# Performance work log

Measured on AMD Instinct MI355X. Metric: run time of the kernel, lower is better.

Reference implementation:

```python
import jax, jax.numpy as jnp
import numpy as np

B = 262144   # number of (group, item) prediction pairs
M = 16       # max members per group (ragged -> padded)
NU = 100000  # num_users
NI = 50000   # num_items
D = 32       # embedding_dim (hardcoded via torch.zeros([32]))


def setup_inputs() -> dict:
    key = jax.random.key(0)
    ks = jax.random.split(key, 9)
    item_inputs = jax.random.randint(ks[0], (B,), 0, NI)
    member_ids = jax.random.randint(ks[1], (B, M), 0, NU)
    lengths = jax.random.randint(ks[2], (B, 1), 1, M + 1)
    member_mask = jnp.arange(M)[None, :] < lengths  # [B, M] bool, variable group sizes
    user_table = jax.random.normal(ks[3], (NU, D), jnp.float32) * 0.1  # xavier-ish
    item_table = jax.random.normal(ks[4], (NI, D), jnp.float32) * 0.1
    W_bil = jax.random.normal(ks[5], (D, D), jnp.float32)  # nn.Bilinear(D, D, 1) weight[0]
    b_bil = jax.random.normal(ks[6], (1,), jnp.float32) * 0.05
    W1 = jax.random.normal(ks[7], (8, 3 * D), jnp.float32) * 0.05  # Linear(96, 8)
    b1 = jnp.zeros((8,), jnp.float32)
    W2 = jax.random.normal(ks[8], (1, 8), jnp.float32) * 0.05  # Linear(8, 1)
    b2 = jnp.zeros((1,), jnp.float32)
    return {
        "item_inputs": item_inputs, "member_ids": member_ids, "member_mask": member_mask,
        "user_table": user_table, "item_table": item_table,
        "W_bil": W_bil, "b_bil": b_bil, "W1": W1, "b1": b1, "W2": W2, "b2": b2,
    }


def reference(item_inputs, member_ids, member_mask, user_table, item_table,
              W_bil, b_bil, W1, b1, W2, b2):
    item_e = item_table[item_inputs]          # [B, D] gather
    mem_e = user_table[member_ids]            # [B, M, D] gather
    # bilinear attention score per member: m^T W i + b (softmax in original is computed then discarded)
    scores = jnp.einsum('bmd,de,be->bm', mem_e, W_bil, item_e) + b_bil[0]
    w = scores * member_mask.astype(scores.dtype)  # zero out padded members (ragged groups)
    final_user = jnp.einsum('bm,bmd->bd', w, mem_e)  # unnormalized weighted sum of members
    new_embeds = jnp.concatenate([final_user * item_e, final_user, item_e], axis=-1)  # [B, 3D]
    h = jax.nn.relu(new_embeds @ W1.T + b1)
    y = jax.nn.sigmoid(h @ W2.T + b2)          # [B, 1]
    return y
```

## Files before the change

### kernel.cpp

```cpp
#include <hip/hip_runtime.h>
#include <math.h>

#define DD 32
#define MM 16

__device__ __forceinline__ void load8f4(const float* __restrict__ p, float* r) {
    const float4* q = (const float4*)p;
#pragma unroll
    for (int i = 0; i < 8; ++i) {
        float4 v = q[i];
        r[4*i+0] = v.x; r[4*i+1] = v.y; r[4*i+2] = v.z; r[4*i+3] = v.w;
    }
}

__global__ void precompute_item(const float* __restrict__ item_table,
                                const float* __restrict__ W_bil,
                                const float* __restrict__ W1,
                                float* __restrict__ tbl, int NI) {
    int i = blockIdx.x * blockDim.x + threadIdx.x;
    if (i >= NI) return;
    float it[DD];
    load8f4(item_table + (size_t)i * DD, it);
    float* o = tbl + (size_t)i * 40;
#pragma unroll 4
    for (int d = 0; d < DD; ++d) {
        float s = 0.f;
#pragma unroll
        for (int e = 0; e < DD; ++e) s = fmaf(W_bil[d * DD + e], it[e], s);
        o[d] = s;
    }
#pragma unroll
    for (int j = 0; j < 8; ++j) {
        float s = 0.f;
#pragma unroll
        for (int d = 0; d < DD; ++d) s = fmaf(W1[j * 96 + 64 + d], it[d], s);
        o[32 + j] = s;
    }
}

template <bool USE_TBL>
__global__ void bilinear_main(const int* __restrict__ item_inputs,
                              const int* __restrict__ member_ids,
                              const unsigned char* __restrict__ member_mask,
                              const float* __restrict__ user_table,
                              const float* __restrict__ item_table,
                              const float* __restrict__ tbl,
                              const float* __restrict__ W_bil,
                              const float* __restrict__ b_bil,
                              const float* __restrict__ W1,
                              const float* __restrict__ b1,
                              const float* __restrict__ W2,
                              const float* __restrict__ b2,
                              float* __restrict__ out, int Btot) {
    int b = blockIdx.x * blockDim.x + threadIdx.x;
    if (b >= Btot) return;

    int item = item_inputs[b];

    uint4 mv = *(const uint4*)(member_mask + (size_t)b * MM);
    int len = __popc(mv.x & 0x01010101u) + __popc(mv.y & 0x01010101u) +
              __popc(mv.z & 0x01010101u) + __popc(mv.w & 0x01010101u);

    int ids[MM];
    {
        const int4* mp = (const int4*)(member_ids + (size_t)b * MM);
#pragma unroll
        for (int q = 0; q < 4; ++q) {
            int4 v = mp[q];
            ids[4*q+0] = v.x; ids[4*q+1] = v.y; ids[4*q+2] = v.z; ids[4*q+3] = v.w;
        }
    }

    float t[DD];
    float cj[8];
    if (USE_TBL) {
        const float* tb = tbl + (size_t)item * 40;
        load8f4(tb, t);
        float4 c0 = *(const float4*)(tb + 32);
        float4 c1 = *(const float4*)(tb + 36);
        cj[0] = c0.x; cj[1] = c0.y; cj[2] = c0.z; cj[3] = c0.w;
        cj[4] = c1.x; cj[5] = c1.y; cj[6] = c1.z; cj[7] = c1.w;
    } else {
        float it0[DD];
        load8f4(item_table + (size_t)item * DD, it0);
#pragma unroll 4
        for (int d = 0; d < DD; ++d) {
            float s = 0.f;
#pragma unroll
            for (int e = 0; e < DD; ++e) s = fmaf(W_bil[d * DD + e], it0[e], s);
            t[d] = s;
        }
#pragma unroll
        for (int j = 0; j < 8; ++j) {
            float s = 0.f;
#pragma unroll
            for (int d = 0; d < DD; ++d) s = fmaf(W1[j * 96 + 64 + d], it0[d], s);
            cj[j] = s;
        }
    }

    float bb = b_bil[0];
    float fin[DD];
#pragma unroll
    for (int d = 0; d < DD; ++d) fin[d] = 0.f;

    for (int m = 0; m < len; ++m) {
        float me[DD];
        load8f4(user_table + (size_t)ids[m] * DD, me);
        float s = bb;
#pragma unroll
        for (int d = 0; d < DD; ++d) s = fmaf(me[d], t[d], s);
#pragma unroll
        for (int d = 0; d < DD; ++d) fin[d] = fmaf(s, me[d], fin[d]);
    }

    float it[DD];
    load8f4(item_table + (size_t)item * DD, it);

    float h[8];
#pragma unroll
    for (int j = 0; j < 8; ++j) h[j] = cj[j] + b1[j];
#pragma unroll
    for (int d = 0; d < DD; ++d) {
        float f = fin[d];
        float p = f * it[d];
#pragma unroll
        for (int j = 0; j < 8; ++j) {
            h[j] = fmaf(W1[j * 96 + d], p, h[j]);
            h[j] = fmaf(W1[j * 96 + 32 + d], f, h[j]);
        }
    }
    float z = b2[0];
#pragma unroll
    for (int j = 0; j < 8; ++j) {
        float hv = h[j] > 0.f ? h[j] : 0.f;
        z = fmaf(W2[j], hv, z);
    }
    out[b] = 1.f / (1.f + __expf(-z));
}

extern "C" void kernel_launch(void* const* d_in, const int* in_sizes, int n_in,
                              void* d_out, int out_size, void* d_ws, size_t ws_size,
                              hipStream_t stream) {
    const int*           item_inputs = (const int*)d_in[0];
    const int*           member_ids  = (const int*)d_in[1];
    const unsigned char* member_mask = (const unsigned char*)d_in[2];
    const float*         user_table  = (const float*)d_in[3];
    const float*         item_table  = (const float*)d_in[4];
    const float*         W_bil       = (const float*)d_in[5];
    const float*         b_bil       = (const float*)d_in[6];
    const float*         W1          = (const float*)d_in[7];
    const float*         b1          = (const float*)d_in[8];
    const float*         W2          = (const float*)d_in[9];
    const float*         b2          = (const float*)d_in[10];
    float* out = (float*)d_out;

    int Btot = in_sizes[0];
    int NI   = in_sizes[4] / DD;

    bool use_tbl = ws_size >= (size_t)NI * 40 * sizeof(float);
    int blk = 256;
    if (use_tbl) {
        float* tbl = (float*)d_ws;
        precompute_item<<<(NI + blk - 1) / blk, blk, 0, stream>>>(item_table, W_bil, W1, tbl, NI);
        bilinear_main<true><<<(Btot + blk - 1) / blk, blk, 0, stream>>>(
            item_inputs, member_ids, member_mask, user_table, item_table, tbl,
            W_bil, b_bil, W1, b1, W2, b2, out, Btot);
    } else {
        bilinear_main<false><<<(Btot + blk - 1) / blk, blk, 0, stream>>>(
            item_inputs, member_ids, member_mask, user_table, item_table, nullptr,
            W_bil, b_bil, W1, b1, W2, b2, out, Btot);
    }
}
```

Before: 142.4 us.

## Parallelize item precompute per dim, pack item rows, unroll member loop by two

The item precompute kernel now uses one thread per (item, dim) instead of one thread per item, which spreads its work over many more threads. The precomputed row grows to 72 floats and also stores a copy of the item embedding, so the main kernel reads one contiguous row instead of also touching item_table. The member loop handles two members per iteration, issuing both gathers before the math to expose more memory-level parallelism, and dot products use four partial accumulators to shorten dependency chains. The trade-offs are a larger workspace table and higher register pressure in the main kernel.

```diff
diff --git a/kernel.cpp b/kernel.cpp
--- a/kernel.cpp
+++ b/kernel.cpp
@@ -3,6 +3,7 @@
 
 #define DD 32
 #define MM 16
+#define TROW 72
 
 __device__ __forceinline__ void load8f4(const float* __restrict__ p, float* r) {
     const float4* q = (const float4*)p;
@@ -17,41 +18,98 @@
                                 const float* __restrict__ W_bil,
                                 const float* __restrict__ W1,
                                 float* __restrict__ tbl, int NI) {
-    int i = blockIdx.x * blockDim.x + threadIdx.x;
-    if (i >= NI) return;
+    int g = blockIdx.x * blockDim.x + threadIdx.x;
+    if (g >= NI * DD) return;
+    int i = g >> 5;
+    int d = g & (DD - 1);
     float it[DD];
     load8f4(item_table + (size_t)i * DD, it);
-    float* o = tbl + (size_t)i * 40;
-#pragma unroll 4
-    for (int d = 0; d < DD; ++d) {
-        float s = 0.f;
-#pragma unroll
-        for (int e = 0; e < DD; ++e) s = fmaf(W_bil[d * DD + e], it[e], s);
-        o[d] = s;
-    }
-#pragma unroll
-    for (int j = 0; j < 8; ++j) {
-        float s = 0.f;
-#pragma unroll
-        for (int d = 0; d < DD; ++d) s = fmaf(W1[j * 96 + 64 + d], it[d], s);
-        o[32 + j] = s;
-    }
+    const float* w = W_bil + d * DD;
+    float s0 = 0.f, s1 = 0.f, s2 = 0.f, s3 = 0.f;
+#pragma unroll
+    for (int e = 0; e < DD; e += 4) {
+        s0 = fmaf(w[e+0], it[e+0], s0);
+        s1 = fmaf(w[e+1], it[e+1], s1);
+        s2 = fmaf(w[e+2], it[e+2], s2);
+        s3 = fmaf(w[e+3], it[e+3], s3);
+    }
+    float* o = tbl + (size_t)i * TROW;
+    o[d]      = (s0 + s1) + (s2 + s3);
+    o[DD + d] = it[d];
+    if (d < 8) {
+        const float* w1 = W1 + d * 96 + 64;
+        float c0 = 0.f, c1 = 0.f, c2 = 0.f, c3 = 0.f;
+#pragma unroll
+        for (int e = 0; e < DD; e += 4) {
+            c0 = fmaf(w1[e+0], it[e+0], c0);
+            c1 = fmaf(w1[e+1], it[e+1], c1);
+            c2 = fmaf(w1[e+2], it[e+2], c2);
+            c3 = fmaf(w1[e+3], it[e+3], c3);
+        }
+        o[64 + d] = (c0 + c1) + (c2 + c3);
+    }
+}
+
+__device__ __forceinline__ void member1(const float* __restrict__ ut, int id,
+                                        const float* __restrict__ t, float bb,
+                                        float* __restrict__ fin) {
+    float me[DD];
+    load8f4(ut + (size_t)id * DD, me);
+    float s0 = 0.f, s1 = 0.f, s2 = 0.f, s3 = 0.f;
+#pragma unroll
+    for (int d = 0; d < DD; d += 4) {
+        s0 = fmaf(me[d+0], t[d+0], s0);
+        s1 = fmaf(me[d+1], t[d+1], s1);
+        s2 = fmaf(me[d+2], t[d+2], s2);
+        s3 = fmaf(me[d+3], t[d+3], s3);
+    }
+    float s = ((s0 + s1) + (s2 + s3)) + bb;
+#pragma unroll
+    for (int d = 0; d < DD; ++d) fin[d] = fmaf(s, me[d], fin[d]);
+}
+
+__device__ __forceinline__ void member2(const float* __restrict__ ut, int ia, int ib,
+                                        const float* __restrict__ t, float bb,
+                                        float* __restrict__ fin) {
+    float ma[DD], mb[DD];
+    load8f4(ut + (size_t)ia * DD, ma);
+    load8f4(ut + (size_t)ib * DD, mb);
+    float a0 = 0.f, a1 = 0.f, a2 = 0.f, a3 = 0.f;
+    float c0 = 0.f, c1 = 0.f, c2 = 0.f, c3 = 0.f;
+#pragma unroll
+    for (int d = 0; d < DD; d += 4) {
+        a0 = fmaf(ma[d+0], t[d+0], a0);
+        a1 = fmaf(ma[d+1], t[d+1], a1);
+        a2 = fmaf(ma[d+2], t[d+2], a2);
+        a3 = fmaf(ma[d+3], t[d+3], a3);
+        c0 = fmaf(mb[d+0], t[d+0], c0);
+        c1 = fmaf(mb[d+1], t[d+1], c1);
+        c2 = fmaf(mb[d+2], t[d+2], c2);
+        c3 = fmaf(mb[d+3], t[d+3], c3);
+    }
+    float sa = ((a0 + a1) + (a2 + a3)) + bb;
+    float sb = ((c0 + c1) + (c2 + c3)) + bb;
+#pragma unroll
+    for (int d = 0; d < DD; ++d) fin[d] = fmaf(sa, ma[d], fin[d]);
+#pragma unroll
+    for (int d = 0; d < DD; ++d) fin[d] = fmaf(sb, mb[d], fin[d]);
 }
 
 template <bool USE_TBL>
-__global__ void bilinear_main(const int* __restrict__ item_inputs,
-                              const int* __restrict__ member_ids,
-                              const unsigned char* __restrict__ member_mask,
-                              const float* __restrict__ user_table,
-                              const float* __restrict__ item_table,
-                              const float* __restrict__ tbl,
-                              const float* __restrict__ W_bil,
-                              const float* __restrict__ b_bil,
-                              const float* __restrict__ W1,
-                              const float* __restrict__ b1,
-                              const float* __restrict__ W2,
-                              const float* __restrict__ b2,
-                              float* __restrict__ out, int Btot) {
+__global__ __launch_bounds__(256)
+void bilinear_main(const int* __restrict__ item_inputs,
+                   const int* __restrict__ member_ids,
+                   const unsigned char* __restrict__ member_mask,
+                   const float* __restrict__ user_table,
+                   const float* __restrict__ item_table,
+                   const float* __restrict__ tbl,
+                   const float* __restrict__ W_bil,
+                   const float* __restrict__ b_bil,
+                   const float* __restrict__ W1,
+                   const float* __restrict__ b1v,
+                   const float* __restrict__ W2,
+                   const float* __restrict__ b2v,
+                   float* __restrict__ out, int Btot) {
     int b = blockIdx.x * blockDim.x + threadIdx.x;
     if (b >= Btot) return;
 
@@ -72,14 +130,10 @@
     }
 
     float t[DD];
-    float cj[8];
+    const float* tb = nullptr;
     if (USE_TBL) {
-        const float* tb = tbl + (size_t)item * 40;
+        tb = tbl + (size_t)item * TROW;
         load8f4(tb, t);
-        float4 c0 = *(const float4*)(tb + 32);
-        float4 c1 = *(const float4*)(tb + 36);
-        cj[0] = c0.x; cj[1] = c0.y; cj[2] = c0.z; cj[3] = c0.w;
-        cj[4] = c1.x; cj[5] = c1.y; cj[6] = c1.z; cj[7] = c1.w;
     } else {
         float it0[DD];
         load8f4(item_table + (size_t)item * DD, it0);
@@ -90,36 +144,41 @@
             for (int e = 0; e < DD; ++e) s = fmaf(W_bil[d * DD + e], it0[e], s);
             t[d] = s;
         }
+    }
+
+    float bb = b_bil[0];
+    float fin[DD];
+#pragma unroll
+    for (int d = 0; d < DD; ++d) fin[d] = 0.f;
+
+    int m = 0;
+    for (; m + 2 <= len; m += 2)
+        member2(user_table, ids[m], ids[m+1], t, bb, fin);
+    if (m < len)
+        member1(user_table, ids[m], t, bb, fin);
+
+    float it[DD];
+    float cj[8];
+    if (USE_TBL) {
+        load8f4(tb + DD, it);
+        float4 q0 = *(const float4*)(tb + 64);
+        float4 q1 = *(const float4*)(tb + 68);
+        cj[0] = q0.x; cj[1] = q0.y; cj[2] = q0.z; cj[3] = q0.w;
+        cj[4] = q1.x; cj[5] = q1.y; cj[6] = q1.z; cj[7] = q1.w;
+    } else {
+        load8f4(item_table + (size_t)item * DD, it);
 #pragma unroll
         for (int j = 0; j < 8; ++j) {
             float s = 0.f;
 #pragma unroll
-            for (int d = 0; d < DD; ++d) s = fmaf(W1[j * 96 + 64 + d], it0[d], s);
+            for (int d = 0; d < DD; ++d) s = fmaf(W1[j * 96 + 64 + d], it[d], s);
             cj[j] = s;
         }
     }
 
-    float bb = b_bil[0];
-    float fin[DD];
-#pragma unroll
-    for (int d = 0; d < DD; ++d) fin[d] = 0.f;
-
-    for (int m = 0; m < len; ++m) {
-        float me[DD];
-        load8f4(user_table + (size_t)ids[m] * DD, me);
-        float s = bb;
-#pragma unroll
-        for (int d = 0; d < DD; ++d) s = fmaf(me[d], t[d], s);
-#pragma unroll
-        for (int d = 0; d < DD; ++d) fin[d] = fmaf(s, me[d], fin[d]);
-    }
-
-    float it[DD];
-    load8f4(item_table + (size_t)item * DD, it);
-
     float h[8];
 #pragma unroll
-    for (int j = 0; j < 8; ++j) h[j] = cj[j] + b1[j];
+    for (int j = 0; j < 8; ++j) h[j] = cj[j] + b1v[j];
 #pragma unroll
     for (int d = 0; d < DD; ++d) {
         float f = fin[d];
@@ -130,7 +189,7 @@
             h[j] = fmaf(W1[j * 96 + 32 + d], f, h[j]);
         }
     }
-    float z = b2[0];
+    float z = b2v[0];
 #pragma unroll
     for (int j = 0; j < 8; ++j) {
         float hv = h[j] > 0.f ? h[j] : 0.f;
@@ -158,11 +217,11 @@
     int Btot = in_sizes[0];
     int NI   = in_sizes[4] / DD;
 
-    bool use_tbl = ws_size >= (size_t)NI * 40 * sizeof(float);
+    bool use_tbl = ws_size >= (size_t)NI * TROW * sizeof(float);
     int blk = 256;
     if (use_tbl) {
         float* tbl = (float*)d_ws;
-        precompute_item<<<(NI + blk - 1) / blk, blk, 0, stream>>>(item_table, W_bil, W1, tbl, NI);
+        precompute_item<<<(NI * DD + blk - 1) / blk, blk, 0, stream>>>(item_table, W_bil, W1, tbl, NI);
         bilinear_main<true><<<(Btot + blk - 1) / blk, blk, 0, stream>>>(
             item_inputs, member_ids, member_mask, user_table, item_table, tbl,
             W_bil, b_bil, W1, b1, W2, b2, out, Btot);
```

After: 167.1 us. +17.3%, slower.

## Split each batch row across four lanes with shuffle reductions

Applied to the files above, without the earlier changes.

Each (group,item) pair is now handled by four threads, each owning an 8-wide slice of the embedding dimension. Partial dot products for attention scores and the first MLP layer are combined with xor shuffles, and one lane finishes the MLP and writes the output with a nontemporal store. This is meant to cut per-thread register use and raise memory-level parallelism for the random user-table gathers, and adjacent lanes now read contiguous 32-byte chunks of the same row. The cost is extra shuffles per member and redundant loads of the ids and mask in every lane.

```diff
diff --git a/kernel.cpp b/kernel.cpp
--- a/kernel.cpp
+++ b/kernel.cpp
@@ -3,6 +3,7 @@
 
 #define DD 32
 #define MM 16
+#define TROW 40
 
 __device__ __forceinline__ void load8f4(const float* __restrict__ p, float* r) {
     const float4* q = (const float4*)p;
@@ -21,7 +22,7 @@
     if (i >= NI) return;
     float it[DD];
     load8f4(item_table + (size_t)i * DD, it);
-    float* o = tbl + (size_t)i * 40;
+    float* o = tbl + (size_t)i * TROW;
 #pragma unroll 4
     for (int d = 0; d < DD; ++d) {
         float s = 0.f;
@@ -39,104 +40,143 @@
 }
 
 template <bool USE_TBL>
-__global__ void bilinear_main(const int* __restrict__ item_inputs,
-                              const int* __restrict__ member_ids,
-                              const unsigned char* __restrict__ member_mask,
-                              const float* __restrict__ user_table,
-                              const float* __restrict__ item_table,
-                              const float* __restrict__ tbl,
-                              const float* __restrict__ W_bil,
-                              const float* __restrict__ b_bil,
-                              const float* __restrict__ W1,
-                              const float* __restrict__ b1,
-                              const float* __restrict__ W2,
-                              const float* __restrict__ b2,
-                              float* __restrict__ out, int Btot) {
-    int b = blockIdx.x * blockDim.x + threadIdx.x;
+__global__ __launch_bounds__(256)
+void bilinear_main(const int* __restrict__ item_inputs,
+                   const int* __restrict__ member_ids,
+                   const unsigned char* __restrict__ member_mask,
+                   const float* __restrict__ user_table,
+                   const float* __restrict__ item_table,
+                   const float* __restrict__ tbl,
+                   const float* __restrict__ W_bil,
+                   const float* __restrict__ b_bil,
+                   const float* __restrict__ W1,
+                   const float* __restrict__ b1v,
+                   const float* __restrict__ W2,
+                   const float* __restrict__ b2v,
+                   float* __restrict__ out, int Btot) {
+    int tid = blockIdx.x * blockDim.x + threadIdx.x;
+    int b = tid >> 2;
     if (b >= Btot) return;
+    int q  = tid & 3;
+    int ko = q * 8;
 
     int item = item_inputs[b];
 
-    uint4 mv = *(const uint4*)(member_mask + (size_t)b * MM);
+    const uint4 mv = *(const uint4*)(member_mask + (size_t)b * MM);
     int len = __popc(mv.x & 0x01010101u) + __popc(mv.y & 0x01010101u) +
               __popc(mv.z & 0x01010101u) + __popc(mv.w & 0x01010101u);
 
-    int ids[MM];
-    {
-        const int4* mp = (const int4*)(member_ids + (size_t)b * MM);
-#pragma unroll
-        for (int q = 0; q < 4; ++q) {
-            int4 v = mp[q];
-            ids[4*q+0] = v.x; ids[4*q+1] = v.y; ids[4*q+2] = v.z; ids[4*q+3] = v.w;
+    float t[8];
+    if (USE_TBL) {
+        const float4* tp = (const float4*)(tbl + (size_t)item * TROW + ko);
+        float4 a = tp[0], c = tp[1];
+        t[0]=a.x; t[1]=a.y; t[2]=a.z; t[3]=a.w; t[4]=c.x; t[5]=c.y; t[6]=c.z; t[7]=c.w;
+    } else {
+        float itf[DD];
+        load8f4(item_table + (size_t)item * DD, itf);
+#pragma unroll
+        for (int k = 0; k < 8; ++k) {
+            const float* w = W_bil + (ko + k) * DD;
+            float s0 = 0.f, s1 = 0.f, s2 = 0.f, s3 = 0.f;
+#pragma unroll
+            for (int e = 0; e < DD; e += 4) {
+                s0 = fmaf(w[e+0], itf[e+0], s0);
+                s1 = fmaf(w[e+1], itf[e+1], s1);
+                s2 = fmaf(w[e+2], itf[e+2], s2);
+                s3 = fmaf(w[e+3], itf[e+3], s3);
+            }
+            t[k] = (s0 + s1) + (s2 + s3);
         }
     }
 
-    float t[DD];
-    float cj[8];
-    if (USE_TBL) {
-        const float* tb = tbl + (size_t)item * 40;
-        load8f4(tb, t);
-        float4 c0 = *(const float4*)(tb + 32);
-        float4 c1 = *(const float4*)(tb + 36);
-        cj[0] = c0.x; cj[1] = c0.y; cj[2] = c0.z; cj[3] = c0.w;
-        cj[4] = c1.x; cj[5] = c1.y; cj[6] = c1.z; cj[7] = c1.w;
-    } else {
-        float it0[DD];
-        load8f4(item_table + (size_t)item * DD, it0);
-#pragma unroll 4
-        for (int d = 0; d < DD; ++d) {
-            float s = 0.f;
-#pragma unroll
-            for (int e = 0; e < DD; ++e) s = fmaf(W_bil[d * DD + e], it0[e], s);
-            t[d] = s;
+    float bb = b_bil[0];
+    float fin[8];
+#pragma unroll
+    for (int k = 0; k < 8; ++k) fin[k] = 0.f;
+
+    const int* idp = member_ids + (size_t)b * MM;
+    int id = idp[0];
+    for (int m = 0; m < len; ++m) {
+        int idn = idp[(m + 1) & (MM - 1)];
+        const float4* up = (const float4*)(user_table + (size_t)id * DD + ko);
+        float4 a = up[0], c = up[1];
+        float me0 = a.x, me1 = a.y, me2 = a.z, me3 = a.w;
+        float me4 = c.x, me5 = c.y, me6 = c.z, me7 = c.w;
+        float s0 = fmaf(me0, t[0], fmaf(me1, t[1], 0.f));
+        float s1 = fmaf(me2, t[2], fmaf(me3, t[3], 0.f));
+        float s2 = fmaf(me4, t[4], fmaf(me5, t[5], 0.f));
+        float s3 = fmaf(me6, t[6], fmaf(me7, t[7], 0.f));
+        float s = (s0 + s1) + (s2 + s3);
+        s += __shfl_xor(s, 1);
+        s += __shfl_xor(s, 2);
+        s += bb;
+        fin[0] = fmaf(s, me0, fin[0]); fin[1] = fmaf(s, me1, fin[1]);
+        fin[2] = fmaf(s, me2, fin[2]); fin[3] = fmaf(s, me3, fin[3]);
+        fin[4] = fmaf(s, me4, fin[4]); fin[5] = fmaf(s, me5, fin[5]);
+        fin[6] = fmaf(s, me6, fin[6]); fin[7] = fmaf(s, me7, fin[7]);
+        id = idn;
+    }
+
+    const float4* ip = (const float4*)(item_table + (size_t)item * DD + ko);
+    float4 ia = ip[0], ic = ip[1];
+    float it8[8] = {ia.x, ia.y, ia.z, ia.w, ic.x, ic.y, ic.z, ic.w};
+
+    float p8[8];
+#pragma unroll
+    for (int k = 0; k < 8; ++k) p8[k] = fin[k] * it8[k];
+
+    float u[8];
+#pragma unroll
+    for (int j = 0; j < 8; ++j) {
+        const float* wr = W1 + j * 96 + ko;
+        float4 wa0 = *(const float4*)(wr);
+        float4 wa1 = *(const float4*)(wr + 4);
+        float4 wb0 = *(const float4*)(wr + 32);
+        float4 wb1 = *(const float4*)(wr + 36);
+        float x = 0.f, y = 0.f;
+        x = fmaf(wa0.x, p8[0], x); y = fmaf(wb0.x, fin[0], y);
+        x = fmaf(wa0.y, p8[1], x); y = fmaf(wb0.y, fin[1], y);
+        x = fmaf(wa0.z, p8[2], x); y = fmaf(wb0.z, fin[2], y);
+        x = fmaf(wa0.w, p8[3], x); y = fmaf(wb0.w, fin[3], y);
+        x = fmaf(wa1.x, p8[4], x); y = fmaf(wb1.x, fin[4], y);
+        x = fmaf(wa1.y, p8[5], x); y = fmaf(wb1.y, fin[5], y);
+        x = fmaf(wa1.z, p8[6], x); y = fmaf(wb1.z, fin[6], y);
+        x = fmaf(wa1.w, p8[7], x); y = fmaf(wb1.w, fin[7], y);
+        u[j] = x + y;
+    }
+#pragma unroll
+    for (int j = 0; j < 8; ++j) {
+        u[j] += __shfl_xor(u[j], 1);
+        u[j] += __shfl_xor(u[j], 2);
+    }
+
+    if (q == 0) {
+        float cj[8];
+        if (USE_TBL) {
+            const float4* cp = (const float4*)(tbl + (size_t)item * TROW + 32);
+            float4 ca = cp[0], cb = cp[1];
+            cj[0]=ca.x; cj[1]=ca.y; cj[2]=ca.z; cj[3]=ca.w;
+            cj[4]=cb.x; cj[5]=cb.y; cj[6]=cb.z; cj[7]=cb.w;
+        } else {
+            float itf[DD];
+            load8f4(item_table + (size_t)item * DD, itf);
+#pragma unroll
+            for (int j = 0; j < 8; ++j) {
+                float s = 0.f;
+#pragma unroll
+                for (int d = 0; d < DD; ++d) s = fmaf(W1[j * 96 + 64 + d], itf[d], s);
+                cj[j] = s;
+            }
         }
+        float z = b2v[0];
 #pragma unroll
         for (int j = 0; j < 8; ++j) {
-            float s = 0.f;
-#pragma unroll
-            for (int d = 0; d < DD; ++d) s = fmaf(W1[j * 96 + 64 + d], it0[d], s);
-            cj[j] = s;
+            float hv = u[j] + cj[j] + b1v[j];
+            hv = hv > 0.f ? hv : 0.f;
+            z = fmaf(W2[j], hv, z);
         }
-    }
-
-    float bb = b_bil[0];
-    float fin[DD];
-#pragma unroll
-    for (int d = 0; d < DD; ++d) fin[d] = 0.f;
-
-    for (int m = 0; m < len; ++m) {
-        float me[DD];
-        load8f4(user_table + (size_t)ids[m] * DD, me);
-        float s = bb;
-#pragma unroll
-        for (int d = 0; d < DD; ++d) s = fmaf(me[d], t[d], s);
-#pragma unroll
-        for (int d = 0; d < DD; ++d) fin[d] = fmaf(s, me[d], fin[d]);
-    }
-
-    float it[DD];
-    load8f4(item_table + (size_t)item * DD, it);
-
-    float h[8];
-#pragma unroll
-    for (int j = 0; j < 8; ++j) h[j] = cj[j] + b1[j];
-#pragma unroll
-    for (int d = 0; d < DD; ++d) {
-        float f = fin[d];
-        float p = f * it[d];
-#pragma unroll
-        for (int j = 0; j < 8; ++j) {
-            h[j] = fmaf(W1[j * 96 + d], p, h[j]);
-            h[j] = fmaf(W1[j * 96 + 32 + d], f, h[j]);
-        }
-    }
-    float z = b2[0];
-#pragma unroll
-    for (int j = 0; j < 8; ++j) {
-        float hv = h[j] > 0.f ? h[j] : 0.f;
-        z = fmaf(W2[j], hv, z);
-    }
-    out[b] = 1.f / (1.f + __expf(-z));
+        __builtin_nontemporal_store(1.f / (1.f + __expf(-z)), out + b);
+    }
 }
 
 extern "C" void kernel_launch(void* const* d_in, const int* in_sizes, int n_in,
@@ -158,16 +198,17 @@
     int Btot = in_sizes[0];
     int NI   = in_sizes[4] / DD;
 
-    bool use_tbl = ws_size >= (size_t)NI * 40 * sizeof(float);
+    bool use_tbl = ws_size >= (size_t)NI * TROW * sizeof(float);
     int blk = 256;
+    long long nthreads = (long long)Btot * 4;
     if (use_tbl) {
         float* tbl = (float*)d_ws;
         precompute_item<<<(NI + blk - 1) / blk, blk, 0, stream>>>(item_table, W_bil, W1, tbl, NI);
-        bilinear_main<true><<<(Btot + blk - 1) / blk, blk, 0, stream>>>(
+        bilinear_main<true><<<(int)((nthreads + blk - 1) / blk), blk, 0, stream>>>(
             item_inputs, member_ids, member_mask, user_table, item_table, tbl,
             W_bil, b_bil, W1, b1, W2, b2, out, Btot);
     } else {
-        bilinear_main<false><<<(Btot + blk - 1) / blk, blk, 0, stream>>>(
+        bilinear_main<false><<<(int)((nthreads + blk - 1) / blk), blk, 0, stream>>>(
             item_inputs, member_ids, member_mask, user_table, item_table, nullptr,
             W_bil, b_bil, W1, b1, W2, b2, out, Btot);
     }
```

Measured after the change: 154.6 us. 1.09x slower.

## Double-buffer member embedding gathers and split item precompute across two threads

Applied to the files above, without the earlier changes.

The member loop now prefetches the next member's embedding row into a second register buffer while the current one is processed, so gather latency overlaps with the dot product and accumulation. Member ids are read directly from global memory rather than preloaded into a register array. The item precompute kernel uses two threads per item, each computing half of the outputs, and dot products use four independent accumulators to shorten FMA dependency chains. The extra buffer raises register pressure, which may reduce occupancy in this latency-bound gather kernel.

```diff
diff --git a/kernel.cpp b/kernel.cpp
--- a/kernel.cpp
+++ b/kernel.cpp
@@ -3,6 +3,7 @@
 
 #define DD 32
 #define MM 16
+#define TROW 40
 
 __device__ __forceinline__ void load8f4(const float* __restrict__ p, float* r) {
     const float4* q = (const float4*)p;
@@ -17,41 +18,70 @@
                                 const float* __restrict__ W_bil,
                                 const float* __restrict__ W1,
                                 float* __restrict__ tbl, int NI) {
-    int i = blockIdx.x * blockDim.x + threadIdx.x;
+    int g = blockIdx.x * blockDim.x + threadIdx.x;
+    int i = g >> 1, h = g & 1;
     if (i >= NI) return;
     float it[DD];
     load8f4(item_table + (size_t)i * DD, it);
-    float* o = tbl + (size_t)i * 40;
-#pragma unroll 4
-    for (int d = 0; d < DD; ++d) {
-        float s = 0.f;
-#pragma unroll
-        for (int e = 0; e < DD; ++e) s = fmaf(W_bil[d * DD + e], it[e], s);
-        o[d] = s;
-    }
-#pragma unroll
-    for (int j = 0; j < 8; ++j) {
-        float s = 0.f;
-#pragma unroll
-        for (int d = 0; d < DD; ++d) s = fmaf(W1[j * 96 + 64 + d], it[d], s);
-        o[32 + j] = s;
-    }
+    float* o = tbl + (size_t)i * TROW;
+    int d0 = h * 16;
+#pragma unroll
+    for (int k = 0; k < 16; ++k) {
+        const float* w = W_bil + (d0 + k) * DD;
+        float s0 = 0.f, s1 = 0.f, s2 = 0.f, s3 = 0.f;
+#pragma unroll
+        for (int e = 0; e < DD; e += 4) {
+            s0 = fmaf(w[e+0], it[e+0], s0);
+            s1 = fmaf(w[e+1], it[e+1], s1);
+            s2 = fmaf(w[e+2], it[e+2], s2);
+            s3 = fmaf(w[e+3], it[e+3], s3);
+        }
+        o[d0 + k] = (s0 + s1) + (s2 + s3);
+    }
+#pragma unroll
+    for (int jj = 0; jj < 4; ++jj) {
+        int j = h * 4 + jj;
+        const float* w1 = W1 + j * 96 + 64;
+        float c0 = 0.f, c1 = 0.f, c2 = 0.f, c3 = 0.f;
+#pragma unroll
+        for (int e = 0; e < DD; e += 4) {
+            c0 = fmaf(w1[e+0], it[e+0], c0);
+            c1 = fmaf(w1[e+1], it[e+1], c1);
+            c2 = fmaf(w1[e+2], it[e+2], c2);
+            c3 = fmaf(w1[e+3], it[e+3], c3);
+        }
+        o[32 + j] = (c0 + c1) + (c2 + c3);
+    }
+}
+
+__device__ __forceinline__ float dot32(const float* __restrict__ a,
+                                       const float* __restrict__ t) {
+    float s0 = 0.f, s1 = 0.f, s2 = 0.f, s3 = 0.f;
+#pragma unroll
+    for (int d = 0; d < DD; d += 4) {
+        s0 = fmaf(a[d+0], t[d+0], s0);
+        s1 = fmaf(a[d+1], t[d+1], s1);
+        s2 = fmaf(a[d+2], t[d+2], s2);
+        s3 = fmaf(a[d+3], t[d+3], s3);
+    }
+    return (s0 + s1) + (s2 + s3);
 }
 
 template <bool USE_TBL>
-__global__ void bilinear_main(const int* __restrict__ item_inputs,
-                              const int* __restrict__ member_ids,
-                              const unsigned char* __restrict__ member_mask,
-                              const float* __restrict__ user_table,
-                              const float* __restrict__ item_table,
-                              const float* __restrict__ tbl,
-                              const float* __restrict__ W_bil,
-                              const float* __restrict__ b_bil,
-                              const float* __restrict__ W1,
-                              const float* __restrict__ b1,
-                              const float* __restrict__ W2,
-                              const float* __restrict__ b2,
-                              float* __restrict__ out, int Btot) {
+__global__ __launch_bounds__(256)
+void bilinear_main(const int* __restrict__ item_inputs,
+                   const int* __restrict__ member_ids,
+                   const unsigned char* __restrict__ member_mask,
+                   const float* __restrict__ user_table,
+                   const float* __restrict__ item_table,
+                   const float* __restrict__ tbl,
+                   const float* __restrict__ W_bil,
+                   const float* __restrict__ b_bil,
+                   const float* __restrict__ W1,
+                   const float* __restrict__ b1v,
+                   const float* __restrict__ W2,
+                   const float* __restrict__ b2v,
+                   float* __restrict__ out, int Btot) {
     int b = blockIdx.x * blockDim.x + threadIdx.x;
     if (b >= Btot) return;
 
@@ -61,20 +91,13 @@
     int len = __popc(mv.x & 0x01010101u) + __popc(mv.y & 0x01010101u) +
               __popc(mv.z & 0x01010101u) + __popc(mv.w & 0x01010101u);
 
-    int ids[MM];
-    {
-        const int4* mp = (const int4*)(member_ids + (size_t)b * MM);
-#pragma unroll
-        for (int q = 0; q < 4; ++q) {
-            int4 v = mp[q];
-            ids[4*q+0] = v.x; ids[4*q+1] = v.y; ids[4*q+2] = v.z; ids[4*q+3] = v.w;
-        }
-    }
+    const int* idp = member_ids + (size_t)b * MM;
 
     float t[DD];
     float cj[8];
+    const float* tb = nullptr;
     if (USE_TBL) {
-        const float* tb = tbl + (size_t)item * 40;
+        tb = tbl + (size_t)item * TROW;
         load8f4(tb, t);
         float4 c0 = *(const float4*)(tb + 32);
         float4 c1 = *(const float4*)(tb + 36);
@@ -104,14 +127,25 @@
 #pragma unroll
     for (int d = 0; d < DD; ++d) fin[d] = 0.f;
 
-    for (int m = 0; m < len; ++m) {
-        float me[DD];
-        load8f4(user_table + (size_t)ids[m] * DD, me);
-        float s = bb;
-#pragma unroll
-        for (int d = 0; d < DD; ++d) s = fmaf(me[d], t[d], s);
-#pragma unroll
-        for (int d = 0; d < DD; ++d) fin[d] = fmaf(s, me[d], fin[d]);
+    float A[DD], Bv[DD];
+    load8f4(user_table + (size_t)idp[0] * DD, A);
+    int m = 0;
+    while (m < len) {
+        if (m + 1 < len) load8f4(user_table + (size_t)idp[m + 1] * DD, Bv);
+        {
+            float s = dot32(A, t) + bb;
+#pragma unroll
+            for (int d = 0; d < DD; ++d) fin[d] = fmaf(s, A[d], fin[d]);
+        }
+        ++m;
+        if (m >= len) break;
+        if (m + 1 < len) load8f4(user_table + (size_t)idp[m + 1] * DD, A);
+        {
+            float s = dot32(Bv, t) + bb;
+#pragma unroll
+            for (int d = 0; d < DD; ++d) fin[d] = fmaf(s, Bv[d], fin[d]);
+        }
+        ++m;
     }
 
     float it[DD];
@@ -119,7 +153,7 @@
 
     float h[8];
 #pragma unroll
-    for (int j = 0; j < 8; ++j) h[j] = cj[j] + b1[j];
+    for (int j = 0; j < 8; ++j) h[j] = cj[j] + b1v[j];
 #pragma unroll
     for (int d = 0; d < DD; ++d) {
         float f = fin[d];
@@ -130,7 +164,7 @@
             h[j] = fmaf(W1[j * 96 + 32 + d], f, h[j]);
         }
     }
-    float z = b2[0];
+    float z = b2v[0];
 #pragma unroll
     for (int j = 0; j < 8; ++j) {
         float hv = h[j] > 0.f ? h[j] : 0.f;
@@ -158,11 +192,11 @@
     int Btot = in_sizes[0];
     int NI   = in_sizes[4] / DD;
 
-    bool use_tbl = ws_size >= (size_t)NI * 40 * sizeof(float);
+    bool use_tbl = ws_size >= (size_t)NI * TROW * sizeof(float);
     int blk = 256;
     if (use_tbl) {
         float* tbl = (float*)d_ws;
-        precompute_item<<<(NI + blk - 1) / blk, blk, 0, stream>>>(item_table, W_bil, W1, tbl, NI);
+        precompute_item<<<(NI * 2 + blk - 1) / blk, blk, 0, stream>>>(item_table, W_bil, W1, tbl, NI);
         bilinear_main<true><<<(Btot + blk - 1) / blk, blk, 0, stream>>>(
             item_inputs, member_ids, member_mask, user_table, item_table, tbl,
             W_bil, b_bil, W1, b1, W2, b2, out, Btot);
```

New measurement: 170.2 us. 1.19x slower.
